# Performance work log

Hardware: AMD Instinct MI355X
Metric: run time of the kernel (lower is better)

The kernel has to match this reference:

```python
import jax, jax.numpy as jnp
import numpy as np

B, T, K, V = 64, 256, 32, 32  # batch, trace_len, net_k, vocab_len


def setup_inputs() -> dict:
    key = jax.random.key(0)
    k1, k2, k3 = jax.random.split(key, 3)
    x = jax.random.uniform(k1, (B, T, V), dtype=jnp.float32)
    w_right = jax.random.normal(k2, (K, K + 1), dtype=jnp.float32)
    w_op = jax.random.normal(k3, (K, 5 + V), dtype=jnp.float32)
    return {"x": x, "w_right": w_right, "w_op": w_op}


def _myrelu(z):
    # CenteredLayer: x<0 -> 0.01*x ; x>1 -> 0.01*x + 0.99 ; else identity
    return jnp.where(z < 0, 0.01 * z, jnp.where(z > 1, 0.01 * z + 0.99, z))


def reference(x, w_right, w_op):
    Bs, Ts, Vs = x.shape
    Ks = w_right.shape[0]
    # cal_softmax()
    sm_op = jax.nn.softmax(w_op, axis=1)
    op_w = sm_op[:, :5].T          # (5, K) operator selection weights
    atom_w = sm_op[:, 5:].T        # (V, K)
    right_w = jax.nn.softmax(w_right, axis=1)[:, :-1].T  # (K, K)

    # atom_x is loop-invariant (x and atom_w do not change across iterations)
    atom_x = jnp.einsum('btv,vk->btk', x, atom_w)  # (B, T, K)
    zcol = jnp.zeros((Bs, Ts, 1), x.dtype)   # last_x (always zeros)
    zrow = jnp.zeros((Bs, 1, Ks), x.dtype)   # end_x  (always zeros)

    def step(all_x, _):
        left = jnp.concatenate([all_x[:, :, 1:], zcol], axis=2)          # shift node dim
        right = jnp.einsum('btk,kj->btj', all_x, right_w)                # right-child mix
        nxt = all_x[:, 1:]                                               # (B, T-1, K)
        X_left = jnp.concatenate(
            [jnp.concatenate([nxt[:, :, 1:], zcol[:, 1:]], axis=2), zrow], axis=1)
        nxt_full = jnp.concatenate([nxt, zrow], axis=1)                  # (B, T, K)
        until = right + _myrelu(left + nxt_full - 1.0)
        new = _myrelu(atom_x
                      + (1.0 - left) * op_w[1]            # not
                      + X_left * op_w[3]                  # next (X)
                      + (left + right - 1.0) * op_w[2]    # and
                      + until * op_w[4])                  # until
        return new, None

    init = jnp.zeros((Bs, Ts, Ks), x.dtype)
    all_x, _ = jax.lax.scan(step, init, None, length=Ts + Ks)
    return jax.nn.sigmoid((all_x - 0.5) * 5.0)
```

## Files before the change

kernel.cpp:

```cpp
#include <hip/hip_runtime.h>
#include <math.h>

#define BB 64
#define TT 256
#define KK 32
#define VV 32
#define CH 64
#define PH 32
#define ROWS (CH + PH)
#define BPB (TT / CH)
#define OWN 12
#define HOLD 16
#define NWAVE (ROWS / OWN)
#define NTHR (NWAVE * 64)
#define NWIN ((TT + KK) / 4)

#define RW_OFF    0
#define WOP_OFF   1024
#define ATOM_OFF  2240
#define STATE_OFF (ATOM_OFF + BB*TT*KK)
#define FLAG_OFF  (STATE_OFF + BB*TT*KK)

typedef __attribute__((ext_vector_type(8))) short short8;
typedef __attribute__((ext_vector_type(4))) float floatx4;
typedef __attribute__((ext_vector_type(4))) int intx4;

__device__ __forceinline__ float myrelu(float z) {
    return fmaf(0.01f, z, 0.99f * __builtin_amdgcn_fmed3f(z, 0.f, 1.f));
}
__device__ __forceinline__ ushort f2bf(float f) {
    union { float f; unsigned int u; } v; v.f = f;
    unsigned int r = v.u + 0x7fffu + ((v.u >> 16) & 1u);
    return (ushort)(r >> 16);
}
__device__ __forceinline__ float dpp_shl1_f(float v) {
    return __int_as_float(__builtin_amdgcn_update_dpp(
        0, __float_as_int(v), 0x101, 0xF, 0xF, true));
}
__device__ __forceinline__ unsigned dpp_shl1_u(unsigned v) {
    return (unsigned)__builtin_amdgcn_update_dpp(
        0, (int)v, 0x101, 0xF, 0xF, true);
}

__global__ void prep_kernel(const float* __restrict__ w_right,
                            const float* __restrict__ w_op,
                            float* __restrict__ ws) {
    int tid = threadIdx.x;
    float* rw  = ws + RW_OFF;
    float* wop = ws + WOP_OFF;
    if (tid < KK) {
        float v[37];
        float m = -1e30f;
        #pragma unroll
        for (int i = 0; i < 37; ++i) { v[i] = w_op[tid * 37 + i]; m = fmaxf(m, v[i]); }
        float s = 0.f;
        #pragma unroll
        for (int i = 0; i < 37; ++i) { v[i] = expf(v[i] - m); s += v[i]; }
        float inv = 1.f / s;
        #pragma unroll
        for (int i = 0; i < 37; ++i) wop[i * KK + tid] = v[i] * inv;
    } else if (tid < 2 * KK) {
        int r = tid - KK;
        float v[KK + 1];
        float m = -1e30f;
        #pragma unroll
        for (int i = 0; i <= KK; ++i) { v[i] = w_right[r * (KK + 1) + i]; m = fmaxf(m, v[i]); }
        float s = 0.f;
        #pragma unroll
        for (int i = 0; i <= KK; ++i) { v[i] = expf(v[i] - m); s += v[i]; }
        float inv = 1.f / s;
        #pragma unroll
        for (int c = 0; c < KK; ++c) rw[c * KK + r] = v[c] * inv;
    }
}

__global__ void atomx_kernel(const float* __restrict__ x, float* __restrict__ ws) {
    const float* aw = ws + WOP_OFF + 5 * KK;
    float* atom = ws + ATOM_OFF;
    int tid = threadIdx.x;
    if (blockIdx.x == 0 && tid < BB * BPB) ((int*)(ws + FLAG_OFF))[tid] = 0;
    int k  = tid & (KK - 1);
    int bt = blockIdx.x * 8 + (tid >> 5);
    const float* xrow = x + bt * VV;
    float acc = 0.f;
    #pragma unroll
    for (int v = 0; v < VV; ++v) acc = fmaf(xrow[v], aw[v * KK + k], acc);
    atom[bt * KK + k] = acc;
}

__global__ __launch_bounds__(NTHR, 1)
void phase_all_kernel(float* __restrict__ ws, float* __restrict__ out) {
    __shared__ float Xe[2][100][36];

    const float* rw   = ws + RW_OFF;
    const float* wop  = ws + WOP_OFF;
    const float* atom = ws + ATOM_OFF;
    float*      state = ws + STATE_OFF;
    int*        flags = (int*)(ws + FLAG_OFF);

    int tid  = threadIdx.x;
    int lane = tid & 63;
    int w    = tid >> 6;
    int lr   = lane & 15;
    int hi   = lane >> 4;
    int b  = blockIdx.x / BPB;
    int c  = blockIdx.x % BPB;
    int lo = c * CH;
    int lrow = w * OWN + lr;
    int t0   = lo + lrow;
    bool active   = (lo + w * OWN) < TT;
    bool straddle = active && (lo + w * OWN + HOLD - 1 >= TT);
    bool tok      = (t0 < TT);
    bool h3       = (hi == 3);

    for (int i = tid; i < 2 * 100 * 36; i += NTHR) (&Xe[0][0][0])[i] = 0.f;

    float* gs = state + (size_t)b * TT * KK;

    float y0 = 0.f, y1 = 0.f, y2 = 0.f, y3 = 0.f;
    float y4 = 0.f, y5 = 0.f, y6 = 0.f, y7 = 0.f;

    floatx4 c0a, c0b;
    float w4c0, w4c1, w4c2, w4c3, w4c4, w4c5, w4c6, w4c7;
    {
        float4 a0 = make_float4(0, 0, 0, 0), a1 = make_float4(0, 0, 0, 0);
        if (tok) {
            a0 = *reinterpret_cast<const float4*>(&atom[((size_t)b * TT + t0) * KK + hi * 8]);
            a1 = *reinterpret_cast<const float4*>(&atom[((size_t)b * TT + t0) * KK + hi * 8 + 4]);
        }
        const float* w1p = wop + 1 * KK + hi * 8;
        const float* w2p = wop + 2 * KK + hi * 8;
        const float* w4p = wop + 4 * KK + hi * 8;
        c0a = (floatx4){a0.x + w1p[0] - w2p[0] - w4p[0],
                        a0.y + w1p[1] - w2p[1] - w4p[1],
                        a0.z + w1p[2] - w2p[2] - w4p[2],
                        a0.w + w1p[3] - w2p[3] - w4p[3]};
        c0b = (floatx4){a1.x + w1p[4] - w2p[4] - w4p[4],
                        a1.y + w1p[5] - w2p[5] - w4p[5],
                        a1.z + w1p[6] - w2p[6] - w4p[6],
                        a1.w + w1p[7] - w2p[7] - w4p[7]};
        w4c0 = 0.99f * w4p[0]; w4c1 = 0.99f * w4p[1];
        w4c2 = 0.99f * w4p[2]; w4c3 = 0.99f * w4p[3];
        w4c4 = 0.99f * w4p[4]; w4c5 = 0.99f * w4p[5];
        w4c6 = 0.99f * w4p[6]; w4c7 = 0.99f * w4p[7];
    }

    short8 af0, af1, nf0, nf1;
    {
        int col0 = ((lr >> 2) << 3) | (lr & 3);
        int col1 = col0 + 4;
        float w1a = wop[1 * KK + col0], w2a = wop[2 * KK + col0];
        float w3a = wop[3 * KK + col0], w4a = wop[4 * KK + col0];
        float w1b = wop[1 * KK + col1], w2b = wop[2 * KK + col1];
        float w3b = wop[3 * KK + col1], w4b = wop[4 * KK + col1];
        float sa = w2a + w4a, sb = w2b + w4b;
        float da = (w2a - w1a) + 0.01f * w4a;
        float db = (w2b - w1b) + 0.01f * w4b;
        const float* rwc0 = rw + col0;
        const float* rwc1 = rw + col1;
        int k0 = hi * 8;
        af0 = (short8){
            (short)f2bf(rwc0[(k0+0)*KK] * sa + ((k0+0 == col0+1) ? da : 0.f)),
            (short)f2bf(rwc0[(k0+1)*KK] * sa + ((k0+1 == col0+1) ? da : 0.f)),
            (short)f2bf(rwc0[(k0+2)*KK] * sa + ((k0+2 == col0+1) ? da : 0.f)),
            (short)f2bf(rwc0[(k0+3)*KK] * sa + ((k0+3 == col0+1) ? da : 0.f)),
            (short)f2bf(rwc0[(k0+4)*KK] * sa + ((k0+4 == col0+1) ? da : 0.f)),
            (short)f2bf(rwc0[(k0+5)*KK] * sa + ((k0+5 == col0+1) ? da : 0.f)),
            (short)f2bf(rwc0[(k0+6)*KK] * sa + ((k0+6 == col0+1) ? da : 0.f)),
            (short)f2bf(rwc0[(k0+7)*KK] * sa + ((k0+7 == col0+1) ? da : 0.f))};
        af1 = (short8){
            (short)f2bf(rwc1[(k0+0)*KK] * sb + ((k0+0 == col1+1) ? db : 0.f)),
            (short)f2bf(rwc1[(k0+1)*KK] * sb + ((k0+1 == col1+1) ? db : 0.f)),
            (short)f2bf(rwc1[(k0+2)*KK] * sb + ((k0+2 == col1+1) ? db : 0.f)),
            (short)f2bf(rwc1[(k0+3)*KK] * sb + ((k0+3 == col1+1) ? db : 0.f)),
            (short)f2bf(rwc1[(k0+4)*KK] * sb + ((k0+4 == col1+1) ? db : 0.f)),
            (short)f2bf(rwc1[(k0+5)*KK] * sb + ((k0+5 == col1+1) ? db : 0.f)),
            (short)f2bf(rwc1[(k0+6)*KK] * sb + ((k0+6 == col1+1) ? db : 0.f)),
            (short)f2bf(rwc1[(k0+7)*KK] * sb + ((k0+7 == col1+1) ? db : 0.f))};
        nf0 = (short8){
            (short)f2bf((k0+0 == col0) ? 0.01f*w4a : ((k0+0 == col0+1) ? w3a : 0.f)),
            (short)f2bf((k0+1 == col0) ? 0.01f*w4a : ((k0+1 == col0+1) ? w3a : 0.f)),
            (short)f2bf((k0+2 == col0) ? 0.01f*w4a : ((k0+2 == col0+1) ? w3a : 0.f)),
            (short)f2bf((k0+3 == col0) ? 0.01f*w4a : ((k0+3 == col0+1) ? w3a : 0.f)),
            (short)f2bf((k0+4 == col0) ? 0.01f*w4a : ((k0+4 == col0+1) ? w3a : 0.f)),
            (short)f2bf((k0+5 == col0) ? 0.01f*w4a : ((k0+5 == col0+1) ? w3a : 0.f)),
            (short)f2bf((k0+6 == col0) ? 0.01f*w4a : ((k0+6 == col0+1) ? w3a : 0.f)),
            (short)f2bf((k0+7 == col0) ? 0.01f*w4a : ((k0+7 == col0+1) ? w3a : 0.f))};
        nf1 = (short8){
            (short)f2bf((k0+0 == col1) ? 0.01f*w4b : ((k0+0 == col1+1) ? w3b : 0.f)),
            (short)f2bf((k0+1 == col1) ? 0.01f*w4b : ((k0+1 == col1+1) ? w3b : 0.f)),
            (short)f2bf((k0+2 == col1) ? 0.01f*w4b : ((k0+2 == col1+1) ? w3b : 0.f)),
            (short)f2bf((k0+3 == col1) ? 0.01f*w4b : ((k0+3 == col1+1) ? w3b : 0.f)),
            (short)f2bf((k0+4 == col1) ? 0.01f*w4b : ((k0+4 == col1+1) ? w3b : 0.f)),
            (short)f2bf((k0+5 == col1) ? 0.01f*w4b : ((k0+5 == col1+1) ? w3b : 0.f)),
            (short)f2bf((k0+6 == col1) ? 0.01f*w4b : ((k0+6 == col1+1) ? w3b : 0.f)),
            (short)f2bf((k0+7 == col1) ? 0.01f*w4b : ((k0+7 == col1+1) ? w3b : 0.f))};
    }

    int pidx = ((lane + 16) & 63) << 2;
    __syncthreads();

    for (int e = 0; e < NWIN; ++e) {
        if (active) {
            #pragma unroll
            for (int s = 0; s < 4; ++s) {
                float nx0 = dpp_shl1_f(y0), nx1 = dpp_shl1_f(y1);
                float nx2 = dpp_shl1_f(y2), nx3 = dpp_shl1_f(y3);
                float nx4 = dpp_shl1_f(y4), nx5 = dpp_shl1_f(y5);
                float nx6 = dpp_shl1_f(y6), nx7 = dpp_shl1_f(y7);
                float lbr = __int_as_float(__builtin_amdgcn_ds_bpermute(pidx, __float_as_int(y0)));
                float lb  = h3 ? 0.f : lbr;

                unsigned bw0, bw1, bw2, bw3;
                asm("v_cvt_pk_bf16_f32 %0, %1, %2" : "=v"(bw0) : "v"(y0), "v"(y1));
                asm("v_cvt_pk_bf16_f32 %0, %1, %2" : "=v"(bw1) : "v"(y2), "v"(y3));
                asm("v_cvt_pk_bf16_f32 %0, %1, %2" : "=v"(bw2) : "v"(y4), "v"(y5));
                asm("v_cvt_pk_bf16_f32 %0, %1, %2" : "=v"(bw3) : "v"(y6), "v"(y7));
                short8 bv = __builtin_bit_cast(short8,
                    (intx4){(int)bw0, (int)bw1, (int)bw2, (int)bw3});
                short8 nv = __builtin_bit_cast(short8,
                    (intx4){(int)dpp_shl1_u(bw0), (int)dpp_shl1_u(bw1),
                            (int)dpp_shl1_u(bw2), (int)dpp_shl1_u(bw3)});

                floatx4 acc0 = __builtin_amdgcn_mfma_f32_16x16x32_bf16(af0, bv, c0a, 0, 0, 0);
                floatx4 acc1 = __builtin_amdgcn_mfma_f32_16x16x32_bf16(af1, bv, c0b, 0, 0, 0);
                acc0 = __builtin_amdgcn_mfma_f32_16x16x32_bf16(nf0, nv, acc0, 0, 0, 0);
                acc1 = __builtin_amdgcn_mfma_f32_16x16x32_bf16(nf1, nv, acc1, 0, 0, 0);

                {
                    float sm = y1 + nx0, t = __builtin_amdgcn_fmed3f(sm, 1.f, 2.f);
                    y0 = myrelu(fmaf(t, w4c0, acc0[0]));
                }
                {
                    float sm = y2 + nx1, t = __builtin_amdgcn_fmed3f(sm, 1.f, 2.f);
                    y1 = myrelu(fmaf(t, w4c1, acc0[1]));
                }
                {
                    float sm = y3 + nx2, t = __builtin_amdgcn_fmed3f(sm, 1.f, 2.f);
                    y2 = myrelu(fmaf(t, w4c2, acc0[2]));
                }
                {
                    float sm = y4 + nx3, t = __builtin_amdgcn_fmed3f(sm, 1.f, 2.f);
                    y3 = myrelu(fmaf(t, w4c3, acc0[3]));
                }
                {
                    float sm = y5 + nx4, t = __builtin_amdgcn_fmed3f(sm, 1.f, 2.f);
                    y4 = myrelu(fmaf(t, w4c4, acc1[0]));
                }
                {
                    float sm = y6 + nx5, t = __builtin_amdgcn_fmed3f(sm, 1.f, 2.f);
                    y5 = myrelu(fmaf(t, w4c5, acc1[1]));
                }
                {
                    float sm = y7 + nx6, t = __builtin_amdgcn_fmed3f(sm, 1.f, 2.f);
                    y6 = myrelu(fmaf(t, w4c6, acc1[2]));
                }
                {
                    float sm = lb + nx7, t = __builtin_amdgcn_fmed3f(sm, 1.f, 2.f);
                    y7 = myrelu(fmaf(t, w4c7, acc1[3]));
                }
                if (straddle && !tok) {
                    y0 = y1 = y2 = y3 = y4 = y5 = y6 = y7 = 0.f;
                }
            }
        }
        if (e == NWIN - 1) break;

        if ((e & 7) == 7) {
            int vv = (e >> 3) + 1;
            if (c > 0 && lr < OWN && lrow < PH) {
                float* gp = gs + (size_t)t0 * KK + hi * 8;
                *reinterpret_cast<float4*>(gp)     = make_float4(y0, y1, y2, y3);
                *reinterpret_cast<float4*>(gp + 4) = make_float4(y4, y5, y6, y7);
            }
            __syncthreads();
            if (tid == 0) {
                if (c > 0) {
                    __threadfence();
                    __hip_atomic_store(&flags[b * BPB + c], vv,
                                       __ATOMIC_RELEASE, __HIP_MEMORY_SCOPE_AGENT);
                }
                if (c < BPB - 1) {
                    while (__hip_atomic_load(&flags[b * BPB + c + 1],
                                             __ATOMIC_ACQUIRE, __HIP_MEMORY_SCOPE_AGENT) < vv)
                        __builtin_amdgcn_s_sleep(2);
                }
            }
            __syncthreads();
            if (lr < OWN && lrow >= CH && tok) {
                unsigned long long* gp =
                    reinterpret_cast<unsigned long long*>(gs + (size_t)t0 * KK + hi * 8);
                unsigned long long u0 = __hip_atomic_load(&gp[0], __ATOMIC_RELAXED, __HIP_MEMORY_SCOPE_AGENT);
                unsigned long long u1 = __hip_atomic_load(&gp[1], __ATOMIC_RELAXED, __HIP_MEMORY_SCOPE_AGENT);
                unsigned long long u2 = __hip_atomic_load(&gp[2], __ATOMIC_RELAXED, __HIP_MEMORY_SCOPE_AGENT);
                unsigned long long u3 = __hip_atomic_load(&gp[3], __ATOMIC_RELAXED, __HIP_MEMORY_SCOPE_AGENT);
                y0 = __uint_as_float((unsigned)u0); y1 = __uint_as_float((unsigned)(u0 >> 32));
                y2 = __uint_as_float((unsigned)u1); y3 = __uint_as_float((unsigned)(u1 >> 32));
                y4 = __uint_as_float((unsigned)u2); y5 = __uint_as_float((unsigned)(u2 >> 32));
                y6 = __uint_as_float((unsigned)u3); y7 = __uint_as_float((unsigned)(u3 >> 32));
            }
        }

        int par = e & 1;
        if (lr < OWN) {
            float* wp = &Xe[par][lrow][hi * 8];
            *reinterpret_cast<float4*>(wp)     = make_float4(y0, y1, y2, y3);
            *reinterpret_cast<float4*>(wp + 4) = make_float4(y4, y5, y6, y7);
        }
        __syncthreads();
        if (lr >= OWN) {
            const float* rp = &Xe[par][lrow][hi * 8];
            float4 v0 = *reinterpret_cast<const float4*>(rp);
            float4 v1 = *reinterpret_cast<const float4*>(rp + 4);
            y0 = v0.x; y1 = v0.y; y2 = v0.z; y3 = v0.w;
            y4 = v1.x; y5 = v1.y; y6 = v1.z; y7 = v1.w;
        }
    }

    if (lr < OWN && lrow < CH) {
        float* op = out + ((size_t)b * TT + t0) * KK + hi * 8;
        float o0 = 1.f / (1.f + __expf(-5.f * (y0 - 0.5f)));
        float o1 = 1.f / (1.f + __expf(-5.f * (y1 - 0.5f)));
        float o2 = 1.f / (1.f + __expf(-5.f * (y2 - 0.5f)));
        float o3 = 1.f / (1.f + __expf(-5.f * (y3 - 0.5f)));
        float o4 = 1.f / (1.f + __expf(-5.f * (y4 - 0.5f)));
        float o5 = 1.f / (1.f + __expf(-5.f * (y5 - 0.5f)));
        float o6 = 1.f / (1.f + __expf(-5.f * (y6 - 0.5f)));
        float o7 = 1.f / (1.f + __expf(-5.f * (y7 - 0.5f)));
        *reinterpret_cast<float4*>(&op[0]) = make_float4(o0, o1, o2, o3);
        *reinterpret_cast<float4*>(&op[4]) = make_float4(o4, o5, o6, o7);
    }
}

extern "C" void kernel_launch(void* const* d_in, const int* in_sizes, int n_in,
                              void* d_out, int out_size, void* d_ws, size_t ws_size,
                              hipStream_t stream) {
    const float* x       = (const float*)d_in[0];
    const float* w_right = (const float*)d_in[1];
    const float* w_op    = (const float*)d_in[2];
    float* ws  = (float*)d_ws;
    float* out = (float*)d_out;

    prep_kernel<<<1, 64, 0, stream>>>(w_right, w_op, ws);
    atomx_kernel<<<BB * TT / 8, 256, 0, stream>>>(x, ws);

    void* args[] = { (void*)&ws, (void*)&out };
    hipLaunchCooperativeKernel((void*)phase_all_kernel,
                               dim3(BB * BPB), dim3(NTHR), args, 0, stream);
}
```

Measured before the change: 225.6 us.

## Replace overlapping-row windows with per-step boundary-row exchange through shared memory

```diff
diff --git a/kernel.cpp b/kernel.cpp
--- a/kernel.cpp
+++ b/kernel.cpp
@@ -8,12 +8,10 @@
 #define CH 64
 #define PH 32
 #define ROWS (CH + PH)
+#define NPHASE ((TT + KK) / PH)
 #define BPB (TT / CH)
-#define OWN 12
-#define HOLD 16
-#define NWAVE (ROWS / OWN)
-#define NTHR (NWAVE * 64)
-#define NWIN ((TT + KK) / 4)
+#define NW (ROWS / 16)
+#define NTHR (NW * 64)
 
 #define RW_OFF    0
 #define WOP_OFF   1024
@@ -36,10 +34,6 @@
 __device__ __forceinline__ float dpp_shl1_f(float v) {
     return __int_as_float(__builtin_amdgcn_update_dpp(
         0, __float_as_int(v), 0x101, 0xF, 0xF, true));
-}
-__device__ __forceinline__ unsigned dpp_shl1_u(unsigned v) {
-    return (unsigned)__builtin_amdgcn_update_dpp(
-        0, (int)v, 0x101, 0xF, 0xF, true);
 }
 
 __global__ void prep_kernel(const float* __restrict__ w_right,
@@ -90,7 +84,7 @@
 
 __global__ __launch_bounds__(NTHR, 1)
 void phase_all_kernel(float* __restrict__ ws, float* __restrict__ out) {
-    __shared__ float Xe[2][100][36];
+    __shared__ float brow[2][NW + 1][36];
 
     const float* rw   = ws + RW_OFF;
     const float* wop  = ws + WOP_OFF;
@@ -100,20 +94,19 @@
 
     int tid  = threadIdx.x;
     int lane = tid & 63;
-    int w    = tid >> 6;
+    int rt   = tid >> 6;
     int lr   = lane & 15;
     int hi   = lane >> 4;
     int b  = blockIdx.x / BPB;
     int c  = blockIdx.x % BPB;
     int lo = c * CH;
-    int lrow = w * OWN + lr;
-    int t0   = lo + lrow;
-    bool active   = (lo + w * OWN) < TT;
-    bool straddle = active && (lo + w * OWN + HOLD - 1 >= TT);
-    bool tok      = (t0 < TT);
-    bool h3       = (hi == 3);
-
-    for (int i = tid; i < 2 * 100 * 36; i += NTHR) (&Xe[0][0][0])[i] = 0.f;
+    int t0 = lo + rt * 16 + lr;
+    bool active = (lo + rt * 16) < TT;
+    bool l15 = (lr == 15);
+    bool h3  = (hi == 3);
+
+    for (int i = tid; i < 2 * (NW + 1) * 36; i += NTHR)
+        (&brow[0][0][0])[i] = 0.f;
 
     float* gs = state + (size_t)b * TT * KK;
 
@@ -124,7 +117,7 @@
     float w4c0, w4c1, w4c2, w4c3, w4c4, w4c5, w4c6, w4c7;
     {
         float4 a0 = make_float4(0, 0, 0, 0), a1 = make_float4(0, 0, 0, 0);
-        if (tok) {
+        if (t0 < TT) {
             a0 = *reinterpret_cast<const float4*>(&atom[((size_t)b * TT + t0) * KK + hi * 8]);
             a1 = *reinterpret_cast<const float4*>(&atom[((size_t)b * TT + t0) * KK + hi * 8 + 4]);
         }
@@ -156,71 +149,50 @@
         float sa = w2a + w4a, sb = w2b + w4b;
         float da = (w2a - w1a) + 0.01f * w4a;
         float db = (w2b - w1b) + 0.01f * w4b;
-        const float* rwc0 = rw + col0;
-        const float* rwc1 = rw + col1;
         int k0 = hi * 8;
-        af0 = (short8){
-            (short)f2bf(rwc0[(k0+0)*KK] * sa + ((k0+0 == col0+1) ? da : 0.f)),
-            (short)f2bf(rwc0[(k0+1)*KK] * sa + ((k0+1 == col0+1) ? da : 0.f)),
-            (short)f2bf(rwc0[(k0+2)*KK] * sa + ((k0+2 == col0+1) ? da : 0.f)),
-            (short)f2bf(rwc0[(k0+3)*KK] * sa + ((k0+3 == col0+1) ? da : 0.f)),
-            (short)f2bf(rwc0[(k0+4)*KK] * sa + ((k0+4 == col0+1) ? da : 0.f)),
-            (short)f2bf(rwc0[(k0+5)*KK] * sa + ((k0+5 == col0+1) ? da : 0.f)),
-            (short)f2bf(rwc0[(k0+6)*KK] * sa + ((k0+6 == col0+1) ? da : 0.f)),
-            (short)f2bf(rwc0[(k0+7)*KK] * sa + ((k0+7 == col0+1) ? da : 0.f))};
-        af1 = (short8){
-            (short)f2bf(rwc1[(k0+0)*KK] * sb + ((k0+0 == col1+1) ? db : 0.f)),
-            (short)f2bf(rwc1[(k0+1)*KK] * sb + ((k0+1 == col1+1) ? db : 0.f)),
-            (short)f2bf(rwc1[(k0+2)*KK] * sb + ((k0+2 == col1+1) ? db : 0.f)),
-            (short)f2bf(rwc1[(k0+3)*KK] * sb + ((k0+3 == col1+1) ? db : 0.f)),
-            (short)f2bf(rwc1[(k0+4)*KK] * sb + ((k0+4 == col1+1) ? db : 0.f)),
-            (short)f2bf(rwc1[(k0+5)*KK] * sb + ((k0+5 == col1+1) ? db : 0.f)),
-            (short)f2bf(rwc1[(k0+6)*KK] * sb + ((k0+6 == col1+1) ? db : 0.f)),
-            (short)f2bf(rwc1[(k0+7)*KK] * sb + ((k0+7 == col1+1) ? db : 0.f))};
-        nf0 = (short8){
-            (short)f2bf((k0+0 == col0) ? 0.01f*w4a : ((k0+0 == col0+1) ? w3a : 0.f)),
-            (short)f2bf((k0+1 == col0) ? 0.01f*w4a : ((k0+1 == col0+1) ? w3a : 0.f)),
-            (short)f2bf((k0+2 == col0) ? 0.01f*w4a : ((k0+2 == col0+1) ? w3a : 0.f)),
-            (short)f2bf((k0+3 == col0) ? 0.01f*w4a : ((k0+3 == col0+1) ? w3a : 0.f)),
-            (short)f2bf((k0+4 == col0) ? 0.01f*w4a : ((k0+4 == col0+1) ? w3a : 0.f)),
-            (short)f2bf((k0+5 == col0) ? 0.01f*w4a : ((k0+5 == col0+1) ? w3a : 0.f)),
-            (short)f2bf((k0+6 == col0) ? 0.01f*w4a : ((k0+6 == col0+1) ? w3a : 0.f)),
-            (short)f2bf((k0+7 == col0) ? 0.01f*w4a : ((k0+7 == col0+1) ? w3a : 0.f))};
-        nf1 = (short8){
-            (short)f2bf((k0+0 == col1) ? 0.01f*w4b : ((k0+0 == col1+1) ? w3b : 0.f)),
-            (short)f2bf((k0+1 == col1) ? 0.01f*w4b : ((k0+1 == col1+1) ? w3b : 0.f)),
-            (short)f2bf((k0+2 == col1) ? 0.01f*w4b : ((k0+2 == col1+1) ? w3b : 0.f)),
-            (short)f2bf((k0+3 == col1) ? 0.01f*w4b : ((k0+3 == col1+1) ? w3b : 0.f)),
-            (short)f2bf((k0+4 == col1) ? 0.01f*w4b : ((k0+4 == col1+1) ? w3b : 0.f)),
-            (short)f2bf((k0+5 == col1) ? 0.01f*w4b : ((k0+5 == col1+1) ? w3b : 0.f)),
-            (short)f2bf((k0+6 == col1) ? 0.01f*w4b : ((k0+6 == col1+1) ? w3b : 0.f)),
-            (short)f2bf((k0+7 == col1) ? 0.01f*w4b : ((k0+7 == col1+1) ? w3b : 0.f))};
+        #pragma unroll
+        for (int q = 0; q < 8; ++q) {
+            int k = k0 + q;
+            af0[q] = (short)f2bf(rw[k * KK + col0] * sa + ((k == col0 + 1) ? da : 0.f));
+            af1[q] = (short)f2bf(rw[k * KK + col1] * sb + ((k == col1 + 1) ? db : 0.f));
+            nf0[q] = (short)f2bf((k == col0) ? 0.01f * w4a : ((k == col0 + 1) ? w3a : 0.f));
+            nf1[q] = (short)f2bf((k == col1) ? 0.01f * w4b : ((k == col1 + 1) ? w3b : 0.f));
+        }
     }
 
     int pidx = ((lane + 16) & 63) << 2;
     __syncthreads();
 
-    for (int e = 0; e < NWIN; ++e) {
-        if (active) {
-            #pragma unroll
-            for (int s = 0; s < 4; ++s) {
+    for (int p = 0; p < NPHASE; ++p) {
+        for (int s = 0; s < PH; ++s) {
+            int cur = s & 1;
+            if (active) {
                 float nx0 = dpp_shl1_f(y0), nx1 = dpp_shl1_f(y1);
                 float nx2 = dpp_shl1_f(y2), nx3 = dpp_shl1_f(y3);
                 float nx4 = dpp_shl1_f(y4), nx5 = dpp_shl1_f(y5);
                 float nx6 = dpp_shl1_f(y6), nx7 = dpp_shl1_f(y7);
+                float4 n0 = *reinterpret_cast<const float4*>(&brow[cur][rt + 1][hi * 8]);
+                float4 n1 = *reinterpret_cast<const float4*>(&brow[cur][rt + 1][hi * 8 + 4]);
+                nx0 = l15 ? n0.x : nx0;  nx1 = l15 ? n0.y : nx1;
+                nx2 = l15 ? n0.z : nx2;  nx3 = l15 ? n0.w : nx3;
+                nx4 = l15 ? n1.x : nx4;  nx5 = l15 ? n1.y : nx5;
+                nx6 = l15 ? n1.z : nx6;  nx7 = l15 ? n1.w : nx7;
                 float lbr = __int_as_float(__builtin_amdgcn_ds_bpermute(pidx, __float_as_int(y0)));
                 float lb  = h3 ? 0.f : lbr;
 
-                unsigned bw0, bw1, bw2, bw3;
+                unsigned bw0, bw1, bw2, bw3, nw0, nw1, nw2, nw3;
                 asm("v_cvt_pk_bf16_f32 %0, %1, %2" : "=v"(bw0) : "v"(y0), "v"(y1));
                 asm("v_cvt_pk_bf16_f32 %0, %1, %2" : "=v"(bw1) : "v"(y2), "v"(y3));
                 asm("v_cvt_pk_bf16_f32 %0, %1, %2" : "=v"(bw2) : "v"(y4), "v"(y5));
                 asm("v_cvt_pk_bf16_f32 %0, %1, %2" : "=v"(bw3) : "v"(y6), "v"(y7));
+                asm("v_cvt_pk_bf16_f32 %0, %1, %2" : "=v"(nw0) : "v"(nx0), "v"(nx1));
+                asm("v_cvt_pk_bf16_f32 %0, %1, %2" : "=v"(nw1) : "v"(nx2), "v"(nx3));
+                asm("v_cvt_pk_bf16_f32 %0, %1, %2" : "=v"(nw2) : "v"(nx4), "v"(nx5));
+                asm("v_cvt_pk_bf16_f32 %0, %1, %2" : "=v"(nw3) : "v"(nx6), "v"(nx7));
                 short8 bv = __builtin_bit_cast(short8,
                     (intx4){(int)bw0, (int)bw1, (int)bw2, (int)bw3});
                 short8 nv = __builtin_bit_cast(short8,
-                    (intx4){(int)dpp_shl1_u(bw0), (int)dpp_shl1_u(bw1),
-                            (int)dpp_shl1_u(bw2), (int)dpp_shl1_u(bw3)});
+                    (intx4){(int)nw0, (int)nw1, (int)nw2, (int)nw3});
 
                 floatx4 acc0 = __builtin_amdgcn_mfma_f32_16x16x32_bf16(af0, bv, c0a, 0, 0, 0);
                 floatx4 acc1 = __builtin_amdgcn_mfma_f32_16x16x32_bf16(af1, bv, c0b, 0, 0, 0);
@@ -259,65 +231,55 @@
                     float sm = lb + nx7, t = __builtin_amdgcn_fmed3f(sm, 1.f, 2.f);
                     y7 = myrelu(fmaf(t, w4c7, acc1[3]));
                 }
-                if (straddle && !tok) {
-                    y0 = y1 = y2 = y3 = y4 = y5 = y6 = y7 = 0.f;
-                }
-            }
-        }
-        if (e == NWIN - 1) break;
-
-        if ((e & 7) == 7) {
-            int vv = (e >> 3) + 1;
-            if (c > 0 && lr < OWN && lrow < PH) {
-                float* gp = gs + (size_t)t0 * KK + hi * 8;
-                *reinterpret_cast<float4*>(gp)     = make_float4(y0, y1, y2, y3);
-                *reinterpret_cast<float4*>(gp + 4) = make_float4(y4, y5, y6, y7);
+
+                if (lr == 0) {
+                    float* wp = &brow[cur ^ 1][rt][hi * 8];
+                    *reinterpret_cast<float4*>(wp)     = make_float4(y0, y1, y2, y3);
+                    *reinterpret_cast<float4*>(wp + 4) = make_float4(y4, y5, y6, y7);
+                }
             }
             __syncthreads();
-            if (tid == 0) {
-                if (c > 0) {
-                    __threadfence();
-                    __hip_atomic_store(&flags[b * BPB + c], vv,
-                                       __ATOMIC_RELEASE, __HIP_MEMORY_SCOPE_AGENT);
-                }
-                if (c < BPB - 1) {
-                    while (__hip_atomic_load(&flags[b * BPB + c + 1],
-                                             __ATOMIC_ACQUIRE, __HIP_MEMORY_SCOPE_AGENT) < vv)
-                        __builtin_amdgcn_s_sleep(2);
-                }
+        }
+        if (p == NPHASE - 1) break;
+
+        if (rt < 2 && c > 0) {
+            float* gp = gs + (size_t)t0 * KK + hi * 8;
+            *reinterpret_cast<float4*>(gp)     = make_float4(y0, y1, y2, y3);
+            *reinterpret_cast<float4*>(gp + 4) = make_float4(y4, y5, y6, y7);
+        }
+        __syncthreads();
+        if (tid == 0) {
+            if (c > 0)
+                __hip_atomic_store(&flags[b * BPB + c], p + 1,
+                                   __ATOMIC_RELEASE, __HIP_MEMORY_SCOPE_AGENT);
+            if (c < BPB - 1) {
+                while (__hip_atomic_load(&flags[b * BPB + c + 1],
+                                         __ATOMIC_ACQUIRE, __HIP_MEMORY_SCOPE_AGENT) < p + 1)
+                    __builtin_amdgcn_s_sleep(2);
             }
-            __syncthreads();
-            if (lr < OWN && lrow >= CH && tok) {
-                unsigned long long* gp =
-                    reinterpret_cast<unsigned long long*>(gs + (size_t)t0 * KK + hi * 8);
-                unsigned long long u0 = __hip_atomic_load(&gp[0], __ATOMIC_RELAXED, __HIP_MEMORY_SCOPE_AGENT);
-                unsigned long long u1 = __hip_atomic_load(&gp[1], __ATOMIC_RELAXED, __HIP_MEMORY_SCOPE_AGENT);
-                unsigned long long u2 = __hip_atomic_load(&gp[2], __ATOMIC_RELAXED, __HIP_MEMORY_SCOPE_AGENT);
-                unsigned long long u3 = __hip_atomic_load(&gp[3], __ATOMIC_RELAXED, __HIP_MEMORY_SCOPE_AGENT);
-                y0 = __uint_as_float((unsigned)u0); y1 = __uint_as_float((unsigned)(u0 >> 32));
-                y2 = __uint_as_float((unsigned)u1); y3 = __uint_as_float((unsigned)(u1 >> 32));
-                y4 = __uint_as_float((unsigned)u2); y5 = __uint_as_float((unsigned)(u2 >> 32));
-                y6 = __uint_as_float((unsigned)u3); y7 = __uint_as_float((unsigned)(u3 >> 32));
+        }
+        __syncthreads();
+        if (active && rt >= CH / 16) {
+            unsigned long long* gp =
+                reinterpret_cast<unsigned long long*>(gs + (size_t)t0 * KK + hi * 8);
+            unsigned long long u0 = __hip_atomic_load(&gp[0], __ATOMIC_RELAXED, __HIP_MEMORY_SCOPE_AGENT);
+            unsigned long long u1 = __hip_atomic_load(&gp[1], __ATOMIC_RELAXED, __HIP_MEMORY_SCOPE_AGENT);
+            unsigned long long u2 = __hip_atomic_load(&gp[2], __ATOMIC_RELAXED, __HIP_MEMORY_SCOPE_AGENT);
+            unsigned long long u3 = __hip_atomic_load(&gp[3], __ATOMIC_RELAXED, __HIP_MEMORY_SCOPE_AGENT);
+            y0 = __uint_as_float((unsigned)u0); y1 = __uint_as_float((unsigned)(u0 >> 32));
+            y2 = __uint_as_float((unsigned)u1); y3 = __uint_as_float((unsigned)(u1 >> 32));
+            y4 = __uint_as_float((unsigned)u2); y5 = __uint_as_float((unsigned)(u2 >> 32));
+            y6 = __uint_as_float((unsigned)u3); y7 = __uint_as_float((unsigned)(u3 >> 32));
+            if (lr == 0) {
+                float* wp = &brow[0][rt][hi * 8];
+                *reinterpret_cast<float4*>(wp)     = make_float4(y0, y1, y2, y3);
+                *reinterpret_cast<float4*>(wp + 4) = make_float4(y4, y5, y6, y7);
             }
         }
-
-        int par = e & 1;
-        if (lr < OWN) {
-            float* wp = &Xe[par][lrow][hi * 8];
-            *reinterpret_cast<float4*>(wp)     = make_float4(y0, y1, y2, y3);
-            *reinterpret_cast<float4*>(wp + 4) = make_float4(y4, y5, y6, y7);
-        }
         __syncthreads();
-        if (lr >= OWN) {
-            const float* rp = &Xe[par][lrow][hi * 8];
-            float4 v0 = *reinterpret_cast<const float4*>(rp);
-            float4 v1 = *reinterpret_cast<const float4*>(rp + 4);
-            y0 = v0.x; y1 = v0.y; y2 = v0.z; y3 = v0.w;
-            y4 = v1.x; y5 = v1.y; y6 = v1.z; y7 = v1.w;
-        }
-    }
-
-    if (lr < OWN && lrow < CH) {
+    }
+
+    if (rt < CH / 16) {
         float* op = out + ((size_t)b * TT + t0) * KK + hi * 8;
         float o0 = 1.f / (1.f + __expf(-5.f * (y0 - 0.5f)));
         float o1 = 1.f / (1.f + __expf(-5.f * (y1 - 0.5f)));
```

Result: slower. 232.5 us (+3.1%).
